# Optimization experiments

Measured on AMD Instinct MI355X. Metric: run time of the kernel, lower is better.

## Reference

```python
import jax, jax.numpy as jnp
import numpy as np


def setup_inputs() -> dict:
    key = jax.random.key(0)
    k_x, k_w, k_b = jax.random.split(key, 3)
    B, Cin, H, W = 32, 256, 56, 56
    Cout, KH, KW = 256, 3, 3
    x = jax.random.normal(k_x, (B, Cin, H, W), dtype=jnp.float32)
    fp_weight = jax.random.normal(k_w, (Cout, Cin, KH, KW), dtype=jnp.float32)
    # binary quantization, conv_mode='input_ch': per-output-channel scale
    scaling_factors = jnp.mean(jnp.abs(fp_weight), axis=(1, 2, 3), keepdims=True)  # [Cout,1,1,1]
    quant_weights = jnp.sign(fp_weight)  # values in {-1,0,1}
    bias = jax.random.normal(k_b, (Cout,), dtype=jnp.float32)
    return {"x": x, "scaling_factors": scaling_factors,
            "quant_weights": quant_weights, "bias": bias}


def reference(x, scaling_factors, quant_weights, bias):
    # Dequantize: per-out-channel scale times sign weights
    new_weights = scaling_factors * quant_weights  # [Cout,Cin,3,3]
    out = jax.lax.conv_general_dilated(
        x, new_weights,
        window_strides=(1, 1),
        padding=((1, 1), (1, 1)),
        dimension_numbers=("NCHW", "OIHW", "NCHW"),
    )
    return out + bias[None, :, None, None]
```

## Files before the change

kernel.cpp:

```cpp
#include <hip/hip_runtime.h>

using half8   = __attribute__((ext_vector_type(8))) _Float16;
using floatx4 = __attribute__((ext_vector_type(4))) float;

__global__ void repack_weights(const float* __restrict__ qw,
                               _Float16* __restrict__ wre, int n) {
  int t = blockIdx.x * 256 + threadIdx.x;
  if (t >= n) return;
  int c  = t & 255;
  int co = (t >> 8) & 255;
  int s  = t >> 16;
  wre[t] = (_Float16)qw[(co * 256 + c) * 9 + s];
}

__global__ __launch_bounds__(256, 2) void binconv_mfma(
    const float* __restrict__ x,
    const float* __restrict__ scale,
    const float* __restrict__ bias,
    const _Float16* __restrict__ wre,
    float* __restrict__ out)
{
  __shared__ _Float16 xs[4 * 58 * 32];

  const int tid  = threadIdx.x;
  const int nb   = blockIdx.x;
  const int b    = nb / 28;
  const int h0   = (nb % 28) * 2;
  const int wave = tid >> 6;
  const int lane = tid & 63;
  const int nl   = lane & 15;
  const int quad = lane >> 4;
  const int co_wave = wave * 64;

  {
    int c = tid & 31;
    int g = tid >> 5;
    int r = g >> 1;
    int side = g & 1;
    xs[(r * 58 + side * 57) * 32 + c] = (_Float16)0.0f;
  }

  int bbase[7];
#pragma unroll
  for (int j = 0; j < 7; ++j) {
    int n = j * 16 + nl;
    int r = (n >= 56) ? 1 : 0;
    int w = n - r * 56;
    bbase[j] = (r * 58 + w) * 64 + quad * 16;
  }

  const _Float16* aptr[4];
#pragma unroll
  for (int mi = 0; mi < 4; ++mi)
    aptr[mi] = wre + (co_wave + mi * 16 + nl) * 256 + quad * 8;

  floatx4 acc[4][7];
#pragma unroll
  for (int mi = 0; mi < 4; ++mi)
#pragma unroll
    for (int j = 0; j < 7; ++j)
      acc[mi][j] = (floatx4){0.f, 0.f, 0.f, 0.f};

  const int sc = tid & 31;
  const int sg = tid >> 5;

  for (int c0 = 0; c0 < 256; c0 += 32) {
    for (int p = sg; p < 28; p += 8) {
      int r  = p / 7;
      int wg = p - r * 7;
      int h  = h0 - 1 + r;
      int w0 = wg * 8;
      float v[8];
      if (h >= 0 && h < 56) {
        const float* src = x + (((long)b * 256 + c0 + sc) * 56 + h) * 56 + w0;
        float4 u0 = *reinterpret_cast<const float4*>(src);
        float4 u1 = *reinterpret_cast<const float4*>(src + 4);
        v[0] = u0.x; v[1] = u0.y; v[2] = u0.z; v[3] = u0.w;
        v[4] = u1.x; v[5] = u1.y; v[6] = u1.z; v[7] = u1.w;
      } else {
#pragma unroll
        for (int i = 0; i < 8; ++i) v[i] = 0.f;
      }
      int basei = (r * 58 + 1 + w0) * 32 + sc;
#pragma unroll
      for (int i = 0; i < 8; ++i) {
        int j = (i + sg) & 7;
        xs[basei + j * 32] = (_Float16)v[j];
      }
    }
    __syncthreads();

#pragma unroll
    for (int s = 0; s < 9; ++s) {
      const int kh = s / 3, kw = s - kh * 3;
      half8 a[4];
#pragma unroll
      for (int mi = 0; mi < 4; ++mi)
        a[mi] = *reinterpret_cast<const half8*>(aptr[mi] + s * 65536 + c0);
      const int soff = (kh * 58 + kw) * 64;
#pragma unroll
      for (int j = 0; j < 7; ++j) {
        half8 bf = *reinterpret_cast<const half8*>(
            reinterpret_cast<const char*>(xs) + bbase[j] + soff);
#pragma unroll
        for (int mi = 0; mi < 4; ++mi)
          acc[mi][j] = __builtin_amdgcn_mfma_f32_16x16x32_f16(a[mi], bf, acc[mi][j], 0, 0, 0);
      }
    }
    __syncthreads();
  }

#pragma unroll
  for (int mi = 0; mi < 4; ++mi) {
#pragma unroll
    for (int reg = 0; reg < 4; ++reg) {
      int co = co_wave + mi * 16 + quad * 4 + reg;
      float s_ = scale[co];
      float bi = bias[co];
#pragma unroll
      for (int j = 0; j < 7; ++j) {
        int n = j * 16 + nl;
        int r = (n >= 56) ? 1 : 0;
        int w = n - r * 56;
        out[(((long)b * 256 + co) * 56 + (h0 + r)) * 56 + w] =
            acc[mi][j][reg] * s_ + bi;
      }
    }
  }
}

extern "C" void kernel_launch(void* const* d_in, const int* in_sizes, int n_in,
                              void* d_out, int out_size, void* d_ws, size_t ws_size,
                              hipStream_t stream) {
  const float* x     = (const float*)d_in[0];
  const float* scale = (const float*)d_in[1];
  const float* qw    = (const float*)d_in[2];
  const float* bias  = (const float*)d_in[3];
  float* out = (float*)d_out;

  _Float16* wre = (_Float16*)d_ws;

  const int nw = 9 * 256 * 256;
  repack_weights<<<(nw + 255) / 256, 256, 0, stream>>>(qw, wre, nw);

  dim3 grid(896);
  binconv_mfma<<<grid, 256, 0, stream>>>(x, scale, bias, wre, out);
}
```

Before: 373.1 us.

## Pre-transpose input to padded fp16 layout and double-buffer via direct global-to-LDS loads

Adds a prep kernel that converts x to fp16 in a channel-innermost, zero-padded row layout in workspace, fused with the weight repack. The main kernel then streams each 32-channel chunk into LDS with global_load_lds DMA, double-buffering so the next chunk's load overlaps the current MFMA work and one barrier per chunk is dropped. The goal is to remove in-kernel fp32-to-fp16 conversion and scattered LDS stores. The cost is an extra pass over x (read fp32, write fp16) and a dependence on workspace size, with the old path kept as a fallback.

```diff
diff --git a/kernel.cpp b/kernel.cpp
--- a/kernel.cpp
+++ b/kernel.cpp
@@ -2,25 +2,63 @@
 
 using half8   = __attribute__((ext_vector_type(8))) _Float16;
 using floatx4 = __attribute__((ext_vector_type(4))) float;
-
-__global__ void repack_weights(const float* __restrict__ qw,
-                               _Float16* __restrict__ wre, int n) {
-  int t = blockIdx.x * 256 + threadIdx.x;
-  if (t >= n) return;
-  int c  = t & 255;
-  int co = (t >> 8) & 255;
-  int s  = t >> 16;
-  wre[t] = (_Float16)qw[(co * 256 + c) * 9 + s];
+using short8  = __attribute__((ext_vector_type(8))) short;
+
+#define XT_ROW_ELEMS 2560
+#define XT_ROW_BYTES 5120
+#define XT_OFF ((size_t)2 << 20)
+#define XT_BYTES ((size_t)256 * 58 * XT_ROW_BYTES)
+
+__device__ __forceinline__ void dma16(const void* g, void* l) {
+  __builtin_amdgcn_global_load_lds(
+      (const __attribute__((address_space(1))) void*)g,
+      (__attribute__((address_space(3))) void*)l, 16, 0, 0);
+}
+
+__global__ __launch_bounds__(256) void prep_kernel(
+    const float* __restrict__ x, const float* __restrict__ qw,
+    _Float16* __restrict__ wre, _Float16* __restrict__ xt)
+{
+  const int bid = blockIdx.x;
+  const int t = threadIdx.x;
+  if (bid >= 14848) {
+    int idx = (bid - 14848) * 256 + t;
+    int c = idx & 255, co = (idx >> 8) & 255, s = idx >> 16;
+    wre[idx] = (_Float16)qw[(co * 256 + c) * 9 + s];
+    return;
+  }
+  __shared__ _Float16 lt[32 * 57];
+  const int hh = bid % 58;
+  const int bc = bid / 58;
+  const int cc = bc & 7, b = bc >> 3;
+  _Float16* dst = xt + ((size_t)bc * 58 + hh) * XT_ROW_ELEMS;
+  const bool interior = (hh >= 1) && (hh <= 56);
+  if (interior) {
+    const int c = t >> 3, j = t & 7;
+    const float* src = x + (((size_t)(b * 256 + cc * 32 + c)) * 56 + (hh - 1)) * 56 + j * 7;
+#pragma unroll
+    for (int i = 0; i < 7; ++i) lt[c * 57 + j * 7 + i] = (_Float16)src[i];
+  }
+  __syncthreads();
+  for (int ch = t; ch < 320; ch += 256) {
+    int pos = ch / 5, sl = ch - pos * 5;
+    short8 v = {0, 0, 0, 0, 0, 0, 0, 0};
+    if (interior && sl < 4 && pos >= 1 && pos <= 56) {
+      int w = pos - 1;
+#pragma unroll
+      for (int i = 0; i < 8; ++i)
+        v[i] = __builtin_bit_cast(short, lt[(sl * 8 + i) * 57 + w]);
+    }
+    *reinterpret_cast<short8*>(dst + ch * 8) = v;
+  }
 }
 
 __global__ __launch_bounds__(256, 2) void binconv_mfma(
-    const float* __restrict__ x,
-    const float* __restrict__ scale,
-    const float* __restrict__ bias,
-    const _Float16* __restrict__ wre,
+    const float* __restrict__ scale, const float* __restrict__ bias,
+    const _Float16* __restrict__ wre, const _Float16* __restrict__ xt,
     float* __restrict__ out)
 {
-  __shared__ _Float16 xs[4 * 58 * 32];
+  __shared__ _Float16 xs[2 * 4 * 64 * 40];
 
   const int tid  = threadIdx.x;
   const int nb   = blockIdx.x;
@@ -32,14 +70,112 @@
   const int quad = lane >> 4;
   const int co_wave = wave * 64;
 
+  int bbase[7];
+#pragma unroll
+  for (int j = 0; j < 7; ++j) {
+    int n = j * 16 + nl;
+    int r = (n >= 56) ? 1 : 0;
+    int w = n - r * 56;
+    bbase[j] = (r * 64 + w) * 80 + quad * 16;
+  }
+
+  const _Float16* aptr[4];
+#pragma unroll
+  for (int mi = 0; mi < 4; ++mi)
+    aptr[mi] = wre + (co_wave + mi * 16 + nl) * 256 + quad * 8;
+
+  floatx4 acc[4][7];
+#pragma unroll
+  for (int mi = 0; mi < 4; ++mi)
+#pragma unroll
+    for (int j = 0; j < 7; ++j)
+      acc[mi][j] = (floatx4){0.f, 0.f, 0.f, 0.f};
+
+  const char* xsrc = (const char*)(xt + ((size_t)(b * 8) * 58 + h0) * XT_ROW_ELEMS);
+  const int wlane = wave * XT_ROW_BYTES + lane * 16;
+  const int wldso = wave * XT_ROW_BYTES;
+
+#pragma unroll
+  for (int i = 0; i < 5; ++i)
+    dma16(xsrc + wlane + i * 1024, (char*)xs + wldso + i * 1024);
+
+  int bufoff = 0;
+  for (int cc = 0; cc < 8; ++cc) {
+    __syncthreads();
+    if (cc < 7) {
+      const char* srcn = xsrc + (size_t)(cc + 1) * (58 * XT_ROW_BYTES);
+#pragma unroll
+      for (int i = 0; i < 5; ++i)
+        dma16(srcn + wlane + i * 1024,
+              (char*)xs + (bufoff ^ 20480) + wldso + i * 1024);
+    }
+    const int c0 = cc * 32;
+    const char* xb = (const char*)xs + bufoff;
+#pragma unroll
+    for (int s = 0; s < 9; ++s) {
+      const int kh = s / 3, kw = s - kh * 3;
+      half8 a[4];
+#pragma unroll
+      for (int mi = 0; mi < 4; ++mi)
+        a[mi] = *reinterpret_cast<const half8*>(aptr[mi] + s * 65536 + c0);
+      const int soff = (kh * 64 + kw) * 80;
+#pragma unroll
+      for (int j = 0; j < 7; ++j) {
+        half8 bf = *reinterpret_cast<const half8*>(xb + bbase[j] + soff);
+#pragma unroll
+        for (int mi = 0; mi < 4; ++mi)
+          acc[mi][j] = __builtin_amdgcn_mfma_f32_16x16x32_f16(a[mi], bf, acc[mi][j], 0, 0, 0);
+      }
+    }
+    bufoff ^= 20480;
+  }
+
+#pragma unroll
+  for (int mi = 0; mi < 4; ++mi) {
+#pragma unroll
+    for (int reg = 0; reg < 4; ++reg) {
+      int co = co_wave + mi * 16 + quad * 4 + reg;
+      float s_ = scale[co];
+      float bi = bias[co];
+#pragma unroll
+      for (int j = 0; j < 7; ++j) {
+        int n = j * 16 + nl;
+        int r = (n >= 56) ? 1 : 0;
+        int w = n - r * 56;
+        out[(((size_t)b * 256 + co) * 56 + (h0 + r)) * 56 + w] =
+            acc[mi][j][reg] * s_ + bi;
+      }
+    }
+  }
+}
+
+__global__ void repack_weights(const float* __restrict__ qw,
+                               _Float16* __restrict__ wre, int n) {
+  int t = blockIdx.x * 256 + threadIdx.x;
+  if (t >= n) return;
+  int c = t & 255, co = (t >> 8) & 255, s = t >> 16;
+  wre[t] = (_Float16)qw[(co * 256 + c) * 9 + s];
+}
+
+__global__ __launch_bounds__(256, 2) void binconv_fallback(
+    const float* __restrict__ x, const float* __restrict__ scale,
+    const float* __restrict__ bias, const _Float16* __restrict__ wre,
+    float* __restrict__ out)
+{
+  __shared__ _Float16 xsl[4 * 58 * 32];
+  const int tid = threadIdx.x;
+  const int nb = blockIdx.x;
+  const int b = nb / 28;
+  const int h0 = (nb % 28) * 2;
+  const int wave = tid >> 6;
+  const int lane = tid & 63;
+  const int nl = lane & 15;
+  const int quad = lane >> 4;
+  const int co_wave = wave * 64;
   {
-    int c = tid & 31;
-    int g = tid >> 5;
-    int r = g >> 1;
-    int side = g & 1;
-    xs[(r * 58 + side * 57) * 32 + c] = (_Float16)0.0f;
-  }
-
+    int c = tid & 31, g = tid >> 5, r = g >> 1, side = g & 1;
+    xsl[(r * 58 + side * 57) * 32 + c] = (_Float16)0.0f;
+  }
   int bbase[7];
 #pragma unroll
   for (int j = 0; j < 7; ++j) {
@@ -48,31 +184,22 @@
     int w = n - r * 56;
     bbase[j] = (r * 58 + w) * 64 + quad * 16;
   }
-
   const _Float16* aptr[4];
 #pragma unroll
   for (int mi = 0; mi < 4; ++mi)
     aptr[mi] = wre + (co_wave + mi * 16 + nl) * 256 + quad * 8;
-
   floatx4 acc[4][7];
 #pragma unroll
   for (int mi = 0; mi < 4; ++mi)
 #pragma unroll
-    for (int j = 0; j < 7; ++j)
-      acc[mi][j] = (floatx4){0.f, 0.f, 0.f, 0.f};
-
-  const int sc = tid & 31;
-  const int sg = tid >> 5;
-
+    for (int j = 0; j < 7; ++j) acc[mi][j] = (floatx4){0.f, 0.f, 0.f, 0.f};
+  const int sc = tid & 31, sg = tid >> 5;
   for (int c0 = 0; c0 < 256; c0 += 32) {
     for (int p = sg; p < 28; p += 8) {
-      int r  = p / 7;
-      int wg = p - r * 7;
-      int h  = h0 - 1 + r;
-      int w0 = wg * 8;
+      int r = p / 7, wg = p - r * 7, h = h0 - 1 + r, w0 = wg * 8;
       float v[8];
       if (h >= 0 && h < 56) {
-        const float* src = x + (((long)b * 256 + c0 + sc) * 56 + h) * 56 + w0;
+        const float* src = x + (((size_t)b * 256 + c0 + sc) * 56 + h) * 56 + w0;
         float4 u0 = *reinterpret_cast<const float4*>(src);
         float4 u1 = *reinterpret_cast<const float4*>(src + 4);
         v[0] = u0.x; v[1] = u0.y; v[2] = u0.z; v[3] = u0.w;
@@ -83,13 +210,9 @@
       }
       int basei = (r * 58 + 1 + w0) * 32 + sc;
 #pragma unroll
-      for (int i = 0; i < 8; ++i) {
-        int j = (i + sg) & 7;
-        xs[basei + j * 32] = (_Float16)v[j];
-      }
+      for (int i = 0; i < 8; ++i) xsl[basei + i * 32] = (_Float16)v[i];
     }
     __syncthreads();
-
 #pragma unroll
     for (int s = 0; s < 9; ++s) {
       const int kh = s / 3, kw = s - kh * 3;
@@ -101,7 +224,7 @@
 #pragma unroll
       for (int j = 0; j < 7; ++j) {
         half8 bf = *reinterpret_cast<const half8*>(
-            reinterpret_cast<const char*>(xs) + bbase[j] + soff);
+            reinterpret_cast<const char*>(xsl) + bbase[j] + soff);
 #pragma unroll
         for (int mi = 0; mi < 4; ++mi)
           acc[mi][j] = __builtin_amdgcn_mfma_f32_16x16x32_f16(a[mi], bf, acc[mi][j], 0, 0, 0);
@@ -109,7 +232,6 @@
     }
     __syncthreads();
   }
-
 #pragma unroll
   for (int mi = 0; mi < 4; ++mi) {
 #pragma unroll
@@ -122,7 +244,7 @@
         int n = j * 16 + nl;
         int r = (n >= 56) ? 1 : 0;
         int w = n - r * 56;
-        out[(((long)b * 256 + co) * 56 + (h0 + r)) * 56 + w] =
+        out[(((size_t)b * 256 + co) * 56 + (h0 + r)) * 56 + w] =
             acc[mi][j][reg] * s_ + bi;
       }
     }
@@ -140,9 +262,12 @@
 
   _Float16* wre = (_Float16*)d_ws;
 
-  const int nw = 9 * 256 * 256;
-  repack_weights<<<(nw + 255) / 256, 256, 0, stream>>>(qw, wre, nw);
-
-  dim3 grid(896);
-  binconv_mfma<<<grid, 256, 0, stream>>>(x, scale, bias, wre, out);
-}
+  if (ws_size >= XT_OFF + XT_BYTES) {
+    _Float16* xt = (_Float16*)((char*)d_ws + XT_OFF);
+    prep_kernel<<<17152, 256, 0, stream>>>(x, qw, wre, xt);
+    binconv_mfma<<<896, 256, 0, stream>>>(scale, bias, wre, xt, out);
+  } else {
+    repack_weights<<<2304, 256, 0, stream>>>(qw, wre, 9 * 256 * 256);
+    binconv_fallback<<<896, 256, 0, stream>>>(x, scale, bias, wre, out);
+  }
+}
```

After: 332.2 us. 10.9% less time.
